# Kernel tuning notes

Measured on AMD Instinct MI355X. Metric: run time of the kernel, lower is better.

## Reference

```python
import math
import jax, jax.numpy as jnp
import numpy as np

DIM = 256
HEADS = 4
TAU = 1e-3
TOPK = 64


def setup_inputs() -> dict:
    key = jax.random.key(0)
    ks = jax.random.split(key, 11)
    B, N, D = 4, 1024, DIM
    s = 1.0 / math.sqrt(D)
    return {
        "F_cls": jax.random.normal(ks[0], (B, N, D), jnp.float32),
        "F_seg": jax.random.normal(ks[1], (B, N, D), jnp.float32),
        "F_age": jax.random.normal(ks[2], (B, N, D), jnp.float32),
        "Wq": jax.random.normal(ks[3], (D, D), jnp.float32) * s,
        "bq": jnp.zeros((D,), jnp.float32),
        "Wk": jax.random.normal(ks[4], (D, D), jnp.float32) * s,
        "bk": jnp.zeros((D,), jnp.float32),
        "Wv": jax.random.normal(ks[5], (D, D), jnp.float32) * s,
        "bv": jnp.zeros((D,), jnp.float32),
        "Wo": jax.random.normal(ks[6], (D, D), jnp.float32) * s,
        "bo": jnp.zeros((D,), jnp.float32),
    }


def reference(F_cls, F_seg, F_age, Wq, bq, Wk, bk, Wv, bv, Wo, bo):
    # Concatenate the three task branches along tokens: (B, 3N, D)
    X = jnp.concatenate([F_cls, F_seg, F_age], axis=1)
    # L1 soft-thresholding
    Xs = jnp.sign(X) * jnp.maximum(jnp.abs(X) - TAU, 0.0)
    B, TN, D = Xs.shape
    N = F_cls.shape[1]
    H, Dh = HEADS, D // HEADS
    # per-sample channel saliency and top-k channel mask
    sal = jnp.abs(Xs).mean(axis=1)                      # (B, D)
    _, idx = jax.lax.top_k(sal, TOPK)                   # (B, k)
    mask = jnp.zeros((B, D), bool).at[jnp.arange(B)[:, None], idx].set(True)
    Xt = Xs * mask[:, None, :]                          # (B, TN, D)
    # shared K/V over all tokens; Q over all tokens equals the concat of the
    # three per-branch q_proj outputs (same weights), so one fused attention
    # is mathematically identical to the three original calls.
    Q = Xt @ Wq.T + bq
    K = Xt @ Wk.T + bk
    V = Xt @ Wv.T + bv
    def heads(x):
        return x.reshape(B, TN, H, Dh).transpose(0, 2, 1, 3)  # (B,H,TN,Dh)
    Qh, Kh, Vh = heads(Q), heads(K), heads(V)
    logits = jnp.einsum("bhqd,bhkd->bhqk", Qh, Kh) / math.sqrt(Dh)
    A = jax.nn.softmax(logits, axis=-1)
    out = jnp.einsum("bhqk,bhkd->bhqd", A, Vh)
    out = out.transpose(0, 2, 1, 3).reshape(B, TN, D)
    out = out @ Wo.T + bo
    return (out[:, 0:N], out[:, N:2 * N], out[:, 2 * N:3 * N])
```

## Files before the change

### kernel.cpp

```cpp
#include <hip/hip_runtime.h>
#include <math.h>

typedef __attribute__((ext_vector_type(8))) short bf16x8;
typedef __attribute__((ext_vector_type(16))) float f32x16;

#define Bsz 4
#define Nn 1024
#define TN 3072
#define Dd 256
#define Hh 4
#define DH 64
#define TAUc 1e-3f
#define QSCALE 0.1803368801111f

#define SALP_OFF 0
#define IDX_OFF  98304
#define XCB_OFF  98560
#define WCT_OFF  491776
#define QB_OFF   590080
#define KB_OFF   2162944
#define VT_OFF   3735808
#define OP0_OFF  5308672
#define OP1_OFF  8454400
#define SML_OFF  11600128

__device__ __forceinline__ ushort f2b(float f) {
    uint u = __float_as_uint(f);
    u += 0x7fffu + ((u >> 16) & 1u);
    return (ushort)(u >> 16);
}
__device__ __forceinline__ uint pk2(float a, float b) {
    return (uint)f2b(a) | ((uint)f2b(b) << 16);
}
__device__ __forceinline__ uint trunc_pk(float a, float b) {
    return (__float_as_uint(a) >> 16) | (__float_as_uint(b) & 0xFFFF0000u);
}
__device__ __forceinline__ float hi_f(float a) {
    return __uint_as_float(__float_as_uint(a) & 0xFFFF0000u);
}
__device__ __forceinline__ uint cvtpk(float a, float b) {
    uint r;
    asm("v_cvt_pk_bf16_f32 %0, %1, %2" : "=v"(r) : "v"(a), "v"(b));
    return r;
}
__device__ __forceinline__ void gld16(const ushort* g, ushort* l) {
    __builtin_amdgcn_global_load_lds(
        (const __attribute__((address_space(1))) uint*)g,
        (__attribute__((address_space(3))) uint*)l, 16, 0, 0);
}
union U4B8 { uint u[4]; bf16x8 v; };
__device__ __forceinline__ bf16x8 ld8(const ushort* p) { return *(const bf16x8*)p; }

__global__ __launch_bounds__(256) void k_sal(
        const float* __restrict__ F0, const float* __restrict__ F1,
        const float* __restrict__ F2, float* __restrict__ salp) {
    int b = blockIdx.x / 96;
    int slab = blockIdx.x - b * 96;
    int t0 = slab * 32;
    int seg = t0 >> 10, tt0 = t0 & 1023;
    const float* F = (seg == 0) ? F0 : (seg == 1 ? F1 : F2);
    const float* base = &F[(size_t)((b << 10) + tt0) * Dd + threadIdx.x];
    float acc = 0.f;
    #pragma unroll 4
    for (int r = 0; r < 32; ++r) {
        float x = base[(size_t)r * Dd];
        acc += fmaxf(fabsf(x) - TAUc, 0.f);
    }
    salp[blockIdx.x * 256 + threadIdx.x] = acc;
}

__global__ void k_topk(const float* __restrict__ salp, int* __restrict__ idx) {
    __shared__ float v[256];
    __shared__ int cnt;
    int b = blockIdx.x, tid = threadIdx.x;
    float myval = 0.f;
    const float* p = &salp[(size_t)b * 96 * 256 + tid];
    #pragma unroll 4
    for (int s = 0; s < 96; ++s) myval += p[s * 256];
    v[tid] = myval;
    if (tid == 0) cnt = 0;
    __syncthreads();
    for (int k = 2; k <= 256; k <<= 1)
        for (int j = k >> 1; j > 0; j >>= 1) {
            int ixj = tid ^ j;
            if (ixj > tid) {
                float a = v[tid], c = v[ixj];
                bool up = ((tid & k) == 0);
                if ((a > c) == up) { v[tid] = c; v[ixj] = a; }
            }
            __syncthreads();
        }
    float thr = v[192];
    if (myval >= thr) {
        int p2 = atomicAdd(&cnt, 1);
        if (p2 < 64) idx[b * 64 + p2] = tid;
    }
}

__global__ __launch_bounds__(256) void k_gather(
        const float* __restrict__ F0, const float* __restrict__ F1,
        const float* __restrict__ F2,
        const float* __restrict__ Wq, const float* __restrict__ Wk,
        const float* __restrict__ Wv, const int* __restrict__ idx,
        uint* __restrict__ Xcb, uint* __restrict__ Wct) {
    __shared__ float xs[32 * 260];
    __shared__ int ids[64];
    int tid = threadIdx.x;
    if (blockIdx.x < 384) {
        int b = blockIdx.x / 96;
        int t0 = (blockIdx.x - b * 96) * 32;
        if (tid < 64) ids[tid] = idx[b * 64 + tid];
        int seg = t0 >> 10, tt0 = t0 & 1023;
        const float* F = (seg == 0) ? F0 : (seg == 1 ? F1 : F2);
        const float* base = &F[(size_t)((b << 10) + tt0) * Dd];
        #pragma unroll
        for (int i = 0; i < 8; ++i) {
            int i0 = tid + i * 256;
            int r = i0 >> 6, c4 = (i0 & 63) << 2;
            float4 x = *(const float4*)&base[(size_t)r * Dd + c4];
            x.x = copysignf(fmaxf(fabsf(x.x) - TAUc, 0.f), x.x);
            x.y = copysignf(fmaxf(fabsf(x.y) - TAUc, 0.f), x.y);
            x.z = copysignf(fmaxf(fabsf(x.z) - TAUc, 0.f), x.z);
            x.w = copysignf(fmaxf(fabsf(x.w) - TAUc, 0.f), x.w);
            *(float4*)&xs[r * 260 + c4] = x;
        }
        __syncthreads();
        #pragma unroll
        for (int i = 0; i < 4; ++i) {
            int i0 = tid + i * 256;
            int r = i0 >> 5, jp = i0 & 31;
            float x0 = xs[r * 260 + ids[2 * jp]];
            float x1 = xs[r * 260 + ids[2 * jp + 1]];
            Xcb[(size_t)(b * TN + t0 + r) * 32 + jp] = pk2(x0, x1);
        }
    } else {
        int gid = (blockIdx.x - 384) * 256 + tid;
        int b = gid / 24576;
        if (tid < 64) ids[tid] = idx[b * 64 + tid];
        __syncthreads();
        int rem = gid - b * 24576;
        int mat = rem / 8192;
        int rem2 = rem - mat * 8192;
        int dout = rem2 >> 5, jp = rem2 & 31;
        const float* Wm = (mat == 0) ? Wq : (mat == 1 ? Wk : Wv);
        float w0 = Wm[(size_t)dout * 256 + ids[2 * jp]];
        float w1 = Wm[(size_t)dout * 256 + ids[2 * jp + 1]];
        Wct[((size_t)(b * 3 + mat) * 256 + dout) * 32 + jp] = pk2(w0, w1);
    }
}

__global__ __launch_bounds__(256) void k_qkv(
        const ushort* __restrict__ Xcb, const ushort* __restrict__ Wct,
        const float* __restrict__ bq, const float* __restrict__ bk,
        const float* __restrict__ bv,
        ushort* __restrict__ Qh, ushort* __restrict__ Kh, ushort* __restrict__ Vt) {
    int wave = threadIdx.x >> 6, lane = threadIdx.x & 63;
    int l31 = lane & 31, h = lane >> 5;
    int W = blockIdx.x * 4 + wave;
    int b = W / 576;
    int r = W - b * 576;
    int mat = r / 192;
    int p = r - mat * 192;
    const ushort* Xb = Xcb + (size_t)b * TN * 64;
    const ushort* Wm = Wct + (size_t)(b * 3 + mat) * 256 * 64;
    f32x16 c[4];
    #pragma unroll
    for (int nt = 0; nt < 4; ++nt)
        #pragma unroll
        for (int q = 0; q < 16; ++q) c[nt][q] = 0.f;
    if (mat < 2) {
        int mtt = p % 96, ng = p / 96;
        const ushort* arow = &Xb[(size_t)(mtt * 32 + l31) * 64];
        #pragma unroll
        for (int kc = 0; kc < 4; ++kc) {
            bf16x8 af = ld8(arow + kc * 16 + 8 * h);
            #pragma unroll
            for (int nt = 0; nt < 4; ++nt) {
                bf16x8 bf = ld8(&Wm[(size_t)(ng * 128 + nt * 32 + l31) * 64 + kc * 16 + 8 * h]);
                c[nt] = __builtin_amdgcn_mfma_f32_32x32x16_bf16(af, bf, c[nt], 0, 0, 0);
            }
        }
        if (mat == 0) {
            #pragma unroll
            for (int nt = 0; nt < 4; ++nt) {
                int dout = ng * 128 + nt * 32 + l31;
                int head = dout >> 6, d63 = dout & 63;
                float bb = bq[dout];
                size_t obase = ((size_t)(b * 4 + head) * TN + mtt * 32) * 64 + d63;
                #pragma unroll
                for (int u = 0; u < 16; ++u) {
                    int trow = (u & 3) + 8 * (u >> 2) + 4 * h;
                    Qh[obase + (size_t)trow * 64] = f2b((c[nt][u] + bb) * QSCALE);
                }
            }
        } else {
            #pragma unroll
            for (int nt = 0; nt < 4; ++nt) {
                int dout = ng * 128 + nt * 32 + l31;
                int head = dout >> 6, d63 = dout & 63;
                float bb = bk[dout];
                size_t base = (size_t)(b * 4 + head) * 196608;
                #pragma unroll
                for (int u = 0; u < 16; ++u) {
                    int trow = (u & 3) + 8 * (u >> 2) + 4 * h;
                    int t = mtt * 32 + trow;
                    int row = t & 127, tile = t >> 7;
                    int fk = (row ^ (row >> 3)) & 7;
                    Kh[base + (size_t)tile * 8192 + row * 64 +
                       (((d63 >> 3) ^ fk) << 3) + (d63 & 7)] = f2b(c[nt][u] + bb);
                }
            }
        }
    } else {
        int mtv = p & 7, tg = p >> 3;
        const ushort* arow = &Wm[(size_t)(mtv * 32 + l31) * 64];
        #pragma unroll
        for (int kc = 0; kc < 4; ++kc) {
            bf16x8 af = ld8(arow + kc * 16 + 8 * h);
            #pragma unroll
            for (int nt = 0; nt < 4; ++nt) {
                bf16x8 bf = ld8(&Xb[(size_t)(tg * 128 + nt * 32 + l31) * 64 + kc * 16 + 8 * h]);
                c[nt] = __builtin_amdgcn_mfma_f32_32x32x16_bf16(af, bf, c[nt], 0, 0, 0);
            }
        }
        int head = mtv >> 1;
        int sl = (l31 & 19) | ((l31 & 4) << 1) | ((l31 & 8) >> 1);
        size_t vbase = (size_t)(b * 4 + head) * 196608 + (size_t)tg * 8192;
        #pragma unroll
        for (int nt = 0; nt < 4; ++nt) {
            int cc = (nt * 32 + sl) >> 3;
            int elem = sl & 7;
            #pragma unroll
            for (int u = 0; u < 16; ++u) {
                int dout = mtv * 32 + (u & 3) + 8 * (u >> 2) + 4 * h;
                int row = dout & 63;
                int fv = (row ^ (row >> 3)) & 7;
                int ch = (cc & 8) | ((cc & 7) ^ fv);
                Vt[vbase + row * 128 + ch * 8 + elem] = f2b(c[nt][u] + bv[dout]);
            }
        }
    }
}

__global__ __launch_bounds__(256, 3) void k_attn(
        const ushort* __restrict__ Qg, const ushort* __restrict__ Kg,
        const ushort* __restrict__ Vtg,
        float* __restrict__ OP0, float* __restrict__ OP1,
        float* __restrict__ Sml) {
    __shared__ __align__(16) ushort Ks[128 * 64];
    __shared__ __align__(16) ushort Vts[64 * 128];
    int bh = blockIdx.x / 48;
    int rem = blockIdx.x - bh * 48;
    int qt = rem >> 1, ks = rem & 1;
    int b = bh >> 2, hh = bh & 3;
    int tid = threadIdx.x, wave = tid >> 6, lane = tid & 63;
    int l31 = lane & 31, h = lane >> 5;
    int q0 = qt * 128 + wave * 32;
    const ushort* Qb = Qg + ((size_t)bh * TN + q0 + l31) * DH;
    bf16x8 qf[4];
    #pragma unroll
    for (int kc = 0; kc < 4; ++kc) qf[kc] = ld8(&Qb[kc * 16 + 8 * h]);

    const ushort* Kt = Kg + (size_t)bh * 196608 + (size_t)(ks * 12) * 8192 + tid * 8;
    const ushort* Vtt = Vtg + (size_t)bh * 196608 + (size_t)(ks * 12) * 8192 + tid * 8;

    f32x16 o0, o1;
    #pragma unroll
    for (int q = 0; q < 16; ++q) { o0[q] = 0.f; o1[q] = 0.f; }
    float lrun = 0.f;

    int fq0 = (l31 ^ (l31 >> 3)) & 7;
    int fq1 = ((32 + l31) ^ ((32 + l31) >> 3)) & 7;

    #pragma unroll 1
    for (int it = 0; it < 12; ++it) {
        __syncthreads();
        #pragma unroll
        for (int i = 0; i < 4; ++i) {
            gld16(Kt + i * 2048, &Ks[(tid + i * 256) * 8]);
            gld16(Vtt + i * 2048, &Vts[(tid + i * 256) * 8]);
        }
        Kt += 8192; Vtt += 8192;
        __syncthreads();

        uint pkA[32];
        float psum = 0.f;
        #pragma unroll
        for (int hf = 0; hf < 2; ++hf) {
            f32x16 s0, s1;
            #pragma unroll
            for (int q = 0; q < 16; ++q) { s0[q] = 0.f; s1[q] = 0.f; }
            int r0 = hf * 64 + l31, r1 = r0 + 32;
            #pragma unroll
            for (int kc = 0; kc < 4; ++kc) {
                int ch = 2 * kc + h;
                bf16x8 k0 = ld8(&Ks[r0 * 64 + ((ch ^ fq0) << 3)]);
                bf16x8 k1 = ld8(&Ks[r1 * 64 + ((ch ^ fq1) << 3)]);
                s0 = __builtin_amdgcn_mfma_f32_32x32x16_bf16(k0, qf[kc], s0, 0, 0, 0);
                s1 = __builtin_amdgcn_mfma_f32_32x32x16_bf16(k1, qf[kc], s1, 0, 0, 0);
            }
            #pragma unroll
            for (int u = 0; u < 8; ++u) {
                float pa = exp2f(s0[2 * u]), pb = exp2f(s0[2 * u + 1]);
                psum += pa + pb;
                pkA[hf * 16 + u] = cvtpk(pa, pb);
            }
            #pragma unroll
            for (int u = 0; u < 8; ++u) {
                float pa = exp2f(s1[2 * u]), pb = exp2f(s1[2 * u + 1]);
                psum += pa + pb;
                pkA[hf * 16 + 8 + u] = cvtpk(pa, pb);
            }
        }
        psum += __shfl_xor(psum, 32);
        lrun += psum;

        #pragma unroll
        for (int kc2 = 0; kc2 < 8; ++kc2) {
            U4B8 pf;
            pf.u[0] = pkA[4 * kc2];     pf.u[1] = pkA[4 * kc2 + 1];
            pf.u[2] = pkA[4 * kc2 + 2]; pf.u[3] = pkA[4 * kc2 + 3];
            int ch = 2 * kc2 + h;
            bf16x8 v0f = ld8(&Vts[l31 * 128 + (((ch & 8) | ((ch & 7) ^ fq0)) << 3)]);
            bf16x8 v1f = ld8(&Vts[(32 + l31) * 128 + (((ch & 8) | ((ch & 7) ^ fq1)) << 3)]);
            o0 = __builtin_amdgcn_mfma_f32_32x32x16_bf16(pf.v, v0f, o0, 0, 0, 0);
            o1 = __builtin_amdgcn_mfma_f32_32x32x16_bf16(pf.v, v1f, o1, 0, 0, 0);
        }
    }

    float* OP = ks ? OP1 : OP0;
    #pragma unroll
    for (int q = 0; q < 16; ++q) {
        int qrow = (q & 3) + 8 * (q >> 2) + 4 * h;
        int t = q0 + qrow;
        size_t base = ((size_t)b * TN + t) * Dd + hh * 64;
        OP[base + l31] = o0[q];
        OP[base + 32 + l31] = o1[q];
    }
    if (h == 0)
        Sml[(size_t)ks * 49152 + (size_t)bh * TN + q0 + l31] = lrun;
}

__global__ __launch_bounds__(256) void k_out(
        const float* __restrict__ OP0, const float* __restrict__ OP1,
        const float* __restrict__ Sml, const float* __restrict__ Wo,
        const float* __restrict__ bo, float* __restrict__ out) {
    __shared__ __align__(16) ushort Ms[2][64][64];
    __shared__ float invsh[64 * 4];
    int nd4 = blockIdx.x;
    int R0 = blockIdx.y * 64;
    int b = R0 / TN;
    int tloc0 = R0 - b * TN;
    int tid = threadIdx.x, wave = tid >> 6, lane = tid & 63;
    int l31 = lane & 31, h = lane >> 5;
    int wt = wave & 1, wd = wave >> 1;
    {
        int hd = tid >> 6, t = tid & 63;
        size_t o = (size_t)(b * 4 + hd) * TN + tloc0 + t;
        invsh[t * 4 + hd] = 1.f / (Sml[o] + Sml[49152 + o]);
    }
    int dout = nd4 * 64 + wd * 32 + l31;
    float bb = bo[dout];
    const float* wrow = &Wo[(size_t)dout * 256];
    int st_t = tid >> 2, st_c = tid & 3;
    int fst = (st_t ^ (st_t >> 3)) & 7;
    size_t gbase = ((size_t)(b * TN + tloc0 + st_t)) * 256 + st_c * 8;
    int trow = wt * 32 + l31;
    int ftr = (trow ^ (trow >> 3)) & 7;
    f32x16 acc;
    #pragma unroll
    for (int q = 0; q < 16; ++q) acc[q] = 0.f;

    auto stage_load = [&](int st, int buf) {
        size_t ob = gbase + (size_t)st * 32;
        float4 x0 = *(const float4*)&OP0[ob];
        float4 x1 = *(const float4*)&OP0[ob + 4];
        float4 y0 = *(const float4*)&OP1[ob];
        float4 y1 = *(const float4*)&OP1[ob + 4];
        float s = invsh[st_t * 4 + (st >> 1)];
        float m0 = (x0.x + y0.x) * s, m1 = (x0.y + y0.y) * s;
        float m2 = (x0.z + y0.z) * s, m3 = (x0.w + y0.w) * s;
        float m4 = (x1.x + y1.x) * s, m5 = (x1.y + y1.y) * s;
        float m6 = (x1.z + y1.z) * s, m7 = (x1.w + y1.w) * s;
        uint4 hi = { trunc_pk(m0, m1), trunc_pk(m2, m3),
                     trunc_pk(m4, m5), trunc_pk(m6, m7) };
        uint4 lo = { trunc_pk(m0 - hi_f(m0), m1 - hi_f(m1)),
                     trunc_pk(m2 - hi_f(m2), m3 - hi_f(m3)),
                     trunc_pk(m4 - hi_f(m4), m5 - hi_f(m5)),
                     trunc_pk(m6 - hi_f(m6), m7 - hi_f(m7)) };
        *(uint4*)&Ms[buf][st_t][(st_c ^ fst) * 8] = hi;
        *(uint4*)&Ms[buf][st_t][((4 + st_c) ^ fst) * 8] = lo;
    };

    __syncthreads();
    stage_load(0, 0);
    #pragma unroll 1
    for (int st = 0; st < 8; ++st) {
        __syncthreads();
        if (st < 7) stage_load(st + 1, (st + 1) & 1);
        int buf = st & 1;
        #pragma unroll
        for (int kc = 0; kc < 2; ++kc) {
            bf16x8 ah = *(const bf16x8*)&Ms[buf][trow][((2 * kc + h) ^ ftr) * 8];
            bf16x8 al = *(const bf16x8*)&Ms[buf][trow][((4 + 2 * kc + h) ^ ftr) * 8];
            int din0 = st * 32 + kc * 16 + 8 * h;
            float4 w0 = *(const float4*)&wrow[din0];
            float4 w1 = *(const float4*)&wrow[din0 + 4];
            U4B8 wh, wl;
            wh.u[0] = trunc_pk(w0.x, w0.y); wh.u[1] = trunc_pk(w0.z, w0.w);
            wh.u[2] = trunc_pk(w1.x, w1.y); wh.u[3] = trunc_pk(w1.z, w1.w);
            wl.u[0] = trunc_pk(w0.x - hi_f(w0.x), w0.y - hi_f(w0.y));
            wl.u[1] = trunc_pk(w0.z - hi_f(w0.z), w0.w - hi_f(w0.w));
            wl.u[2] = trunc_pk(w1.x - hi_f(w1.x), w1.y - hi_f(w1.y));
            wl.u[3] = trunc_pk(w1.z - hi_f(w1.z), w1.w - hi_f(w1.w));
            acc = __builtin_amdgcn_mfma_f32_32x32x16_bf16(ah, wh.v, acc, 0, 0, 0);
            acc = __builtin_amdgcn_mfma_f32_32x32x16_bf16(al, wh.v, acc, 0, 0, 0);
            acc = __builtin_amdgcn_mfma_f32_32x32x16_bf16(ah, wl.v, acc, 0, 0, 0);
        }
    }
    #pragma unroll
    for (int u = 0; u < 16; ++u) {
        int tloc = tloc0 + wt * 32 + (u & 3) + 8 * (u >> 2) + 4 * h;
        int chunk = tloc >> 10, tt = tloc & 1023;
        out[(size_t)chunk * (Bsz * Nn * Dd) + ((size_t)(b * Nn + tt)) * Dd + dout] =
            acc[u] + bb;
    }
}

extern "C" void kernel_launch(void* const* d_in, const int* in_sizes, int n_in,
                              void* d_out, int out_size, void* d_ws, size_t ws_size,
                              hipStream_t stream) {
    const float* F0 = (const float*)d_in[0];
    const float* F1 = (const float*)d_in[1];
    const float* F2 = (const float*)d_in[2];
    const float* Wq = (const float*)d_in[3];
    const float* bq = (const float*)d_in[4];
    const float* Wk = (const float*)d_in[5];
    const float* bk = (const float*)d_in[6];
    const float* Wv = (const float*)d_in[7];
    const float* bv = (const float*)d_in[8];
    const float* Wo = (const float*)d_in[9];
    const float* bo = (const float*)d_in[10];
    float* ws = (float*)d_ws;
    float* out = (float*)d_out;

    int* idxp = (int*)(ws + IDX_OFF);
    uint* Xcb = (uint*)(ws + XCB_OFF);
    uint* Wct = (uint*)(ws + WCT_OFF);
    ushort* Qb16 = (ushort*)(ws + QB_OFF);
    ushort* Kb16 = (ushort*)(ws + KB_OFF);
    ushort* Vt16 = (ushort*)(ws + VT_OFF);
    float* OP0 = ws + OP0_OFF;
    float* OP1 = ws + OP1_OFF;
    float* Sml = ws + SML_OFF;

    k_sal<<<384, 256, 0, stream>>>(F0, F1, F2, ws + SALP_OFF);
    k_topk<<<Bsz, 256, 0, stream>>>(ws + SALP_OFF, idxp);
    k_gather<<<768, 256, 0, stream>>>(F0, F1, F2, Wq, Wk, Wv, idxp, Xcb, Wct);
    k_qkv<<<576, 256, 0, stream>>>((const ushort*)Xcb, (const ushort*)Wct,
                                   bq, bk, bv, Qb16, Kb16, Vt16);
    k_attn<<<768, 256, 0, stream>>>(Qb16, Kb16, Vt16, OP0, OP1, Sml);
    k_out<<<dim3(4, 192), 256, 0, stream>>>(OP0, OP1, Sml, Wo, bo, out);
}
```

Baseline: 186.9 us.

## Double-buffer K/V tiles in attention kernel with 64-key half tiles

The attention kernel now stages K and V in two 64-key LDS buffers and prefetches the next half tile while computing on the current one, replacing the load-sync-compute loop over 128-key tiles. This is meant to overlap global-to-LDS transfer latency with MFMA work and halve the synchronizations per loaded tile. LDS footprint stays the same, but the V tile is re-sliced from the 128-wide transposed layout, so the swizzle and indexing must still match what the earlier stage wrote.

Result: no change. 187.9 us (+0.6%).

```diff
diff --git a/kernel.cpp b/kernel.cpp
--- a/kernel.cpp
+++ b/kernel.cpp
@@ -247,11 +247,11 @@
         const ushort* __restrict__ Vtg,
         float* __restrict__ OP0, float* __restrict__ OP1,
         float* __restrict__ Sml) {
-    __shared__ __align__(16) ushort Ks[128 * 64];
-    __shared__ __align__(16) ushort Vts[64 * 128];
+    __shared__ __align__(16) ushort Ks[2][64 * 64];
+    __shared__ __align__(16) ushort Vts[2][64 * 64];
     int bh = blockIdx.x / 48;
     int rem = blockIdx.x - bh * 48;
-    int qt = rem >> 1, ks = rem & 1;
+    int qt = rem >> 1, ksplit = rem & 1;
     int b = bh >> 2, hh = bh & 3;
     int tid = threadIdx.x, wave = tid >> 6, lane = tid & 63;
     int l31 = lane & 31, h = lane >> 5;
@@ -261,8 +261,12 @@
     #pragma unroll
     for (int kc = 0; kc < 4; ++kc) qf[kc] = ld8(&Qb[kc * 16 + 8 * h]);
 
-    const ushort* Kt = Kg + (size_t)bh * 196608 + (size_t)(ks * 12) * 8192 + tid * 8;
-    const ushort* Vtt = Vtg + (size_t)bh * 196608 + (size_t)(ks * 12) * 8192 + tid * 8;
+    const ushort* Ktb = Kg + (size_t)bh * 196608 + (size_t)ksplit * 98304;
+    const ushort* Vtb = Vtg + (size_t)bh * 196608 + (size_t)ksplit * 98304;
+
+    int koff0 = tid * 8, koff1 = tid * 8 + 2048;
+    int voff0 = (tid >> 3) * 128 + (tid & 7) * 8;
+    int voff1 = voff0 + 4096;
 
     f32x16 o0, o1;
     #pragma unroll
@@ -271,64 +275,71 @@
 
     int fq0 = (l31 ^ (l31 >> 3)) & 7;
     int fq1 = ((32 + l31) ^ ((32 + l31) >> 3)) & 7;
-
-    #pragma unroll 1
-    for (int it = 0; it < 12; ++it) {
-        __syncthreads();
-        #pragma unroll
-        for (int i = 0; i < 4; ++i) {
-            gld16(Kt + i * 2048, &Ks[(tid + i * 256) * 8]);
-            gld16(Vtt + i * 2048, &Vts[(tid + i * 256) * 8]);
-        }
-        Kt += 8192; Vtt += 8192;
-        __syncthreads();
-
-        uint pkA[32];
+    int r0c = l31 * 64, r1c = (32 + l31) * 64;
+
+    auto stage = [&](int ht, ushort* KsD, ushort* VtsD) {
+        const ushort* ksrc = Ktb + (size_t)ht * 4096;
+        const ushort* vsrc = Vtb + (size_t)((ht >> 1) * 8192 + (ht & 1) * 64);
+        gld16(ksrc + koff0, KsD + koff0);
+        gld16(ksrc + koff1, KsD + koff1);
+        gld16(vsrc + voff0, VtsD + koff0);
+        gld16(vsrc + voff1, VtsD + koff1);
+    };
+
+    auto compute = [&](const ushort* KsB, const ushort* VtsB) {
+        f32x16 s0, s1;
+        #pragma unroll
+        for (int q = 0; q < 16; ++q) { s0[q] = 0.f; s1[q] = 0.f; }
+        #pragma unroll
+        for (int kc = 0; kc < 4; ++kc) {
+            int ch = 2 * kc + h;
+            bf16x8 k0 = ld8(&KsB[r0c + ((ch ^ fq0) << 3)]);
+            bf16x8 k1 = ld8(&KsB[r1c + ((ch ^ fq1) << 3)]);
+            s0 = __builtin_amdgcn_mfma_f32_32x32x16_bf16(k0, qf[kc], s0, 0, 0, 0);
+            s1 = __builtin_amdgcn_mfma_f32_32x32x16_bf16(k1, qf[kc], s1, 0, 0, 0);
+        }
+        uint pkA[16];
         float psum = 0.f;
         #pragma unroll
-        for (int hf = 0; hf < 2; ++hf) {
-            f32x16 s0, s1;
-            #pragma unroll
-            for (int q = 0; q < 16; ++q) { s0[q] = 0.f; s1[q] = 0.f; }
-            int r0 = hf * 64 + l31, r1 = r0 + 32;
-            #pragma unroll
-            for (int kc = 0; kc < 4; ++kc) {
-                int ch = 2 * kc + h;
-                bf16x8 k0 = ld8(&Ks[r0 * 64 + ((ch ^ fq0) << 3)]);
-                bf16x8 k1 = ld8(&Ks[r1 * 64 + ((ch ^ fq1) << 3)]);
-                s0 = __builtin_amdgcn_mfma_f32_32x32x16_bf16(k0, qf[kc], s0, 0, 0, 0);
-                s1 = __builtin_amdgcn_mfma_f32_32x32x16_bf16(k1, qf[kc], s1, 0, 0, 0);
-            }
-            #pragma unroll
-            for (int u = 0; u < 8; ++u) {
-                float pa = exp2f(s0[2 * u]), pb = exp2f(s0[2 * u + 1]);
-                psum += pa + pb;
-                pkA[hf * 16 + u] = cvtpk(pa, pb);
-            }
-            #pragma unroll
-            for (int u = 0; u < 8; ++u) {
-                float pa = exp2f(s1[2 * u]), pb = exp2f(s1[2 * u + 1]);
-                psum += pa + pb;
-                pkA[hf * 16 + 8 + u] = cvtpk(pa, pb);
-            }
+        for (int u = 0; u < 8; ++u) {
+            float pa = exp2f(s0[2 * u]), pb = exp2f(s0[2 * u + 1]);
+            psum += pa + pb;
+            pkA[u] = cvtpk(pa, pb);
+        }
+        #pragma unroll
+        for (int u = 0; u < 8; ++u) {
+            float pa = exp2f(s1[2 * u]), pb = exp2f(s1[2 * u + 1]);
+            psum += pa + pb;
+            pkA[8 + u] = cvtpk(pa, pb);
         }
         psum += __shfl_xor(psum, 32);
         lrun += psum;
-
-        #pragma unroll
-        for (int kc2 = 0; kc2 < 8; ++kc2) {
+        #pragma unroll
+        for (int kc2 = 0; kc2 < 4; ++kc2) {
             U4B8 pf;
             pf.u[0] = pkA[4 * kc2];     pf.u[1] = pkA[4 * kc2 + 1];
             pf.u[2] = pkA[4 * kc2 + 2]; pf.u[3] = pkA[4 * kc2 + 3];
             int ch = 2 * kc2 + h;
-            bf16x8 v0f = ld8(&Vts[l31 * 128 + (((ch & 8) | ((ch & 7) ^ fq0)) << 3)]);
-            bf16x8 v1f = ld8(&Vts[(32 + l31) * 128 + (((ch & 8) | ((ch & 7) ^ fq1)) << 3)]);
+            bf16x8 v0f = ld8(&VtsB[r0c + ((ch ^ fq0) << 3)]);
+            bf16x8 v1f = ld8(&VtsB[r1c + ((ch ^ fq1) << 3)]);
             o0 = __builtin_amdgcn_mfma_f32_32x32x16_bf16(pf.v, v0f, o0, 0, 0, 0);
             o1 = __builtin_amdgcn_mfma_f32_32x32x16_bf16(pf.v, v1f, o1, 0, 0, 0);
         }
-    }
-
-    float* OP = ks ? OP1 : OP0;
+    };
+
+    stage(0, Ks[0], Vts[0]);
+    __syncthreads();
+    #pragma unroll 1
+    for (int t = 0; t < 24; t += 2) {
+        stage(t + 1, Ks[1], Vts[1]);
+        compute(Ks[0], Vts[0]);
+        __syncthreads();
+        if (t + 2 < 24) stage(t + 2, Ks[0], Vts[0]);
+        compute(Ks[1], Vts[1]);
+        __syncthreads();
+    }
+
+    float* OP = ksplit ? OP1 : OP0;
     #pragma unroll
     for (int q = 0; q < 16; ++q) {
         int qrow = (q & 3) + 8 * (q >> 2) + 4 * h;
@@ -338,7 +349,7 @@
         OP[base + 32 + l31] = o1[q];
     }
     if (h == 0)
-        Sml[(size_t)ks * 49152 + (size_t)bh * TN + q0 + l31] = lrun;
+        Sml[(size_t)ksplit * 49152 + (size_t)bh * TN + q0 + l31] = lrun;
 }
 
 __global__ __launch_bounds__(256) void k_out(
```
